# Kernel optimization log

Measured on AMD Instinct MI355X. Metric: run time of the kernel, lower is better.

The kernel has to match this reference:

```python
import jax, jax.numpy as jnp
import numpy as np


def _block(x, a, b):
    # [..., W, H, D] -> [..., W//a, H//b, a, b, D]
    w, h, d = x.shape[-3:]
    x = jnp.reshape(x, x.shape[:-3] + (w // a, a, h // b, b, d))
    return jnp.moveaxis(x, -4, -3)


def _combine(x, bs):
    # [..., W, H, D] -> [..., W//bs, H//bs, bs*bs*D]
    x = _block(x, bs, bs)
    return jnp.reshape(x, x.shape[:-3] + (-1,))


def _normalize(x):
    x = x - jnp.mean(x, axis=-1, keepdims=True)
    return x / (jnp.linalg.norm(x, axis=-1, keepdims=True) + 1e-05)


def setup_inputs() -> dict:
    key = jax.random.key(0)
    k1, k2 = jax.random.split(key)
    x = jax.random.normal(k1, (8, 128, 128, 64), dtype=jnp.float32)
    y = jax.random.normal(k2, (8, 128, 128, 64), dtype=jnp.float32)
    return {"x": x, "y": y, "blocksize": 4}


def reference(x, y, blocksize):
    shape = x.shape
    xc = _normalize(_combine(x, blocksize))  # [B, W/bs, H/bs, F]
    yc = _normalize(_combine(y, blocksize))
    yf = jnp.reshape(yc, (-1, yc.shape[-1]))  # [M, F] codebook
    # single similarity matrix, reused for min-loss and argmax (original
    # computed jnp.inner twice -- same math)
    sim = jnp.einsum('...f,mf->...m', xc, yf)  # [B, W/bs, H/bs, M]
    cosloss = jnp.mean(jnp.min(1.0 - sim, axis=-1))
    idx = jnp.argmax(sim, axis=-1)
    # one-hot matmul against yf == top-1 gather (argmax picks first max, as
    # does the original I = (argmax - arange == 0) construction)
    new_x = jnp.take(yf, idx, axis=0)  # [B, W/bs, H/bs, F]
    new_x = jnp.reshape(new_x, new_x.shape[:-1] + (blocksize, blocksize, -1))
    new_x = jnp.swapaxes(new_x, -4, -3)
    new_x = jnp.reshape(new_x, shape)
    return cosloss, new_x
```

## Files before the change

kernel.cpp:

```cpp
#include <hip/hip_runtime.h>
#include <math.h>


#define NROWS 8192
#define KY 1024
#define NCH 32
#define EPS 3e-4f
#define FEPS 8e-4f

typedef _Float16 v8h __attribute__((ext_vector_type(8)));
typedef float f32x4 __attribute__((ext_vector_type(4)));

__device__ __forceinline__ void gload16(const _Float16* g, _Float16* l) {
    __builtin_amdgcn_global_load_lds(
        (const __attribute__((address_space(1))) void*)g,
        (__attribute__((address_space(3))) void*)l, 16, 0, 0);
}

__device__ __forceinline__ unsigned umax(unsigned a, unsigned b) { return a > b ? a : b; }
__device__ __forceinline__ unsigned umin(unsigned a, unsigned b) { return a < b ? a : b; }

__device__ __forceinline__ unsigned packKey(float v, int col) {
    unsigned b = __float_as_uint(v);
    b ^= (unsigned)((int)b >> 31) | 0x80000000u;
    return (b & 0xFFFFE000u) | (unsigned)(8191 - col);
}

__device__ __forceinline__ float unpackApprox(unsigned k) {
    unsigned kb = k & 0xFFFFE000u;
    unsigned b = (kb & 0x80000000u) ? (kb ^ 0x80000000u) : ~kb;
    return __uint_as_float(b);
}

#define KMERGE(a1, a2, a3, b1, b2, b3) do {                                 \
    unsigned _n1 = umax(a1, b1);                                            \
    unsigned _n2 = umax(umin(a1, b1), umax(a2, b2));                        \
    unsigned _n3 = umax(umax(a3, b3), umax(umin(a1, b2), umin(a2, b1)));    \
    a1 = _n1; a2 = _n2; a3 = _n3;                                           \
} while (0)

__global__ __launch_bounds__(256) void normSplitKernel(
    const float* __restrict__ x, const float* __restrict__ y,
    _Float16* __restrict__ Xh, _Float16* __restrict__ Xl,
    _Float16* __restrict__ Yh, _Float16* __restrict__ Yl,
    int* __restrict__ flagCnt) {
    if (blockIdx.x == 0 && threadIdx.x == 0) *flagCnt = 0;
    int gr = blockIdx.x * 4 + (threadIdx.x >> 6);
    int ln = threadIdx.x & 63;
    bool isX = gr < NROWS;
    int row = isX ? gr : gr - NROWS;
    const float* src = isX ? x : y;
    _Float16* dh = isX ? Xh : Yh;
    _Float16* dl = isX ? Xl : Yl;
    int b = row >> 10, wq = (row >> 5) & 31, hq = row & 31;
    int a = ln >> 4, c = (ln >> 2) & 3, d0 = (ln & 3) << 4;
    const float* p = &src[(((size_t)(b * 128) + wq * 4 + a) * 128 + hq * 4 + c) * 64 + d0];
    float vv[16];
    *(float4*)(vv + 0)  = *(const float4*)(p + 0);
    *(float4*)(vv + 4)  = *(const float4*)(p + 4);
    *(float4*)(vv + 8)  = *(const float4*)(p + 8);
    *(float4*)(vv + 12) = *(const float4*)(p + 12);
    double s = 0.0;
    #pragma unroll
    for (int q = 0; q < 16; q++) s += (double)vv[q];
    #pragma unroll
    for (int m = 1; m < 64; m <<= 1) s += __shfl_xor(s, m, 64);
    double mean = s * (1.0 / 1024.0);
    double ss = 0.0;
    #pragma unroll
    for (int q = 0; q < 16; q++) {
        double d = (double)vv[q] - mean;
        ss += d * d;
    }
    #pragma unroll
    for (int m = 1; m < 64; m <<= 1) ss += __shfl_xor(ss, m, 64);
    double scale = 1.0 / (sqrt(ss) + 1e-5);
    _Float16 hi[16], lo[16];
    #pragma unroll
    for (int q = 0; q < 16; q++) {
        float f = (float)(((double)vv[q] - mean) * scale);
        _Float16 h = (_Float16)f;
        hi[q] = h;
        lo[q] = (_Float16)(f - (float)h);
    }
    size_t f0 = (size_t)row * KY + (ln << 4);
    *(v8h*)&dh[f0]     = *(v8h*)(hi);
    *(v8h*)&dh[f0 + 8] = *(v8h*)(hi + 8);
    *(v8h*)&dl[f0]     = *(v8h*)(lo);
    *(v8h*)&dl[f0 + 8] = *(v8h*)(lo + 8);
}

__global__ __launch_bounds__(512, 2) void simKernel(
    const _Float16* __restrict__ Xh, const _Float16* __restrict__ Yh,
    float* __restrict__ pV1, unsigned* __restrict__ pK1,
    unsigned* __restrict__ pK2, unsigned* __restrict__ pK3) {
    __shared__ __align__(16) _Float16 As[2][256 * 32];
    __shared__ __align__(16) _Float16 Bs[2][256 * 32];
    __shared__ unsigned sK[2][4][128][3];
    __shared__ float sE[2][4][128];
    const int t = threadIdx.x;
    const int l = t & 63, w = t >> 6;
    const int wr = w >> 2, wc = w & 3;
    const int quad = l >> 4, lm = l & 15;
    const int flat = blockIdx.x;
    const int bx = flat >> 5, by = flat & 31;
    const int r0 = bx * 256, c0 = by * 256;

    f32x4 acc[8][4];
    #pragma unroll
    for (int i = 0; i < 8; i++)
        #pragma unroll
        for (int j = 0; j < 4; j++) acc[i][j] = (f32x4){0.f, 0.f, 0.f, 0.f};

    const int cq = l >> 2;
    const int sA = (((l & 3) ^ (cq & 3)) << 3);
    const _Float16* gA = Xh + (size_t)(r0 + w * 16 + cq) * KY + sA;
    const _Float16* gB = Yh + (size_t)(c0 + w * 16 + cq) * KY + sA;
    const int ldsBase = w * 512;

#define STAGE(bb, kt) do {                                             \
    const int _ko = (kt) * 32;                                         \
    gload16(gA + _ko,                     &As[bb][ldsBase]);           \
    gload16(gA + _ko + (size_t)128 * KY,  &As[bb][ldsBase + 4096]);    \
    gload16(gB + _ko,                     &Bs[bb][ldsBase]);           \
    gload16(gB + _ko + (size_t)128 * KY,  &Bs[bb][ldsBase + 4096]);    \
} while (0)

    const int swz = (quad ^ (lm & 3)) << 3;
    const int offA0 = (wr * 128 + lm) * 32 + swz;
    const int offB0 = (wc * 64 + lm) * 32 + swz;

    STAGE(0, 0);
    STAGE(1, 1);
    asm volatile("s_waitcnt vmcnt(4)" ::: "memory");
    __builtin_amdgcn_s_barrier();

    #pragma unroll 2
    for (int kt = 0; kt < 32; kt++) {
        const int cur = kt & 1;
        v8h af[8], bf[4];
        #pragma unroll
        for (int i = 0; i < 8; i++) af[i] = *(const v8h*)&As[cur][offA0 + i * 512];
        #pragma unroll
        for (int j = 0; j < 4; j++) bf[j] = *(const v8h*)&Bs[cur][offB0 + j * 512];
        asm volatile("s_waitcnt lgkmcnt(0)" ::: "memory");
        __builtin_amdgcn_sched_barrier(0);
        __builtin_amdgcn_s_barrier();
        STAGE(cur, (kt + 2) & 31);
        __builtin_amdgcn_s_setprio(1);
        #pragma unroll
        for (int j = 0; j < 4; j++)
            #pragma unroll
            for (int i = 0; i < 8; i++)
                acc[i][j] = __builtin_amdgcn_mfma_f32_16x16x32_f16(af[i], bf[j], acc[i][j], 0, 0, 0);
        __builtin_amdgcn_s_setprio(0);
        asm volatile("s_waitcnt vmcnt(4)" ::: "memory");
        __builtin_amdgcn_s_barrier();
    }
    asm volatile("s_waitcnt vmcnt(0)" ::: "memory");
#undef STAGE

    const int cbase = c0 + wc * 64 + lm;
    #pragma unroll
    for (int i = 0; i < 8; i++) {
        #pragma unroll
        for (int r = 0; r < 4; r++) {
            float v0 = acc[i][0][r], v1 = acc[i][1][r];
            float v2 = acc[i][2][r], v3 = acc[i][3][r];
            unsigned k0 = packKey(v0, cbase);
            unsigned k1 = packKey(v1, cbase + 16);
            unsigned k2 = packKey(v2, cbase + 32);
            unsigned k3 = packKey(v3, cbase + 48);
            unsigned h1 = umax(k0, k1), l1 = umin(k0, k1);
            unsigned h2 = umax(k2, k3), l2 = umin(k2, k3);
            unsigned a1 = umax(h1, h2);
            unsigned a2 = umax(umin(h1, h2), umax(l1, l2));
            unsigned a3 = umax(umin(h1, l2), umin(l1, h2));
            float ev = fmaxf(fmaxf(v0, v1), fmaxf(v2, v3));
            #pragma unroll
            for (int m = 1; m < 16; m <<= 1) {
                unsigned b1 = (unsigned)__shfl_xor((int)a1, m, 64);
                unsigned b2 = (unsigned)__shfl_xor((int)a2, m, 64);
                unsigned b3 = (unsigned)__shfl_xor((int)a3, m, 64);
                float be = __shfl_xor(ev, m, 64);
                KMERGE(a1, a2, a3, b1, b2, b3);
                ev = fmaxf(ev, be);
            }
            if (lm == 0) {
                int rr = i * 16 + quad * 4 + r;
                sK[wr][wc][rr][0] = a1; sK[wr][wc][rr][1] = a2; sK[wr][wc][rr][2] = a3;
                sE[wr][wc][rr] = ev;
            }
        }
    }
    __syncthreads();
    if (t < 256) {
        const int mwr = t >> 7, ri = t & 127;
        unsigned a1 = sK[mwr][0][ri][0], a2 = sK[mwr][0][ri][1], a3 = sK[mwr][0][ri][2];
        float ev = sE[mwr][0][ri];
        #pragma unroll
        for (int q = 1; q < 4; q++) {
            unsigned b1 = sK[mwr][q][ri][0], b2 = sK[mwr][q][ri][1], b3 = sK[mwr][q][ri][2];
            KMERGE(a1, a2, a3, b1, b2, b3);
            ev = fmaxf(ev, sE[mwr][q][ri]);
        }
        size_t o = (size_t)by * NROWS + (r0 + t);
        pV1[o] = ev;
        pK1[o] = a1; pK2[o] = a2; pK3[o] = a3;
    }
}

__global__ __launch_bounds__(256) void reduceKernel(
    const float* __restrict__ pV1, const unsigned* __restrict__ pK1,
    const unsigned* __restrict__ pK2, const unsigned* __restrict__ pK3,
    int* __restrict__ bestIdx, int* __restrict__ flagRows,
    int* __restrict__ flagC2, int* __restrict__ flagC3,
    int* __restrict__ flagCnt, float* __restrict__ blkSum) {
    int t = threadIdx.x;
    int g = blockIdx.x * 256 + t;
    int row = g >> 2, sub = g & 3;
    unsigned a1 = 0, a2 = 0, a3 = 0;
    float ev = -1e30f;
    #pragma unroll
    for (int k = 0; k < 8; k++) {
        size_t o = (size_t)(sub + (k << 2)) * NROWS + row;
        unsigned b1 = pK1[o], b2 = pK2[o], b3 = pK3[o];
        float e = pV1[o];
        KMERGE(a1, a2, a3, b1, b2, b3);
        ev = fmaxf(ev, e);
    }
    #pragma unroll
    for (int m = 1; m < 4; m <<= 1) {
        unsigned b1 = (unsigned)__shfl_xor((int)a1, m, 64);
        unsigned b2 = (unsigned)__shfl_xor((int)a2, m, 64);
        unsigned b3 = (unsigned)__shfl_xor((int)a3, m, 64);
        float be = __shfl_xor(ev, m, 64);
        KMERGE(a1, a2, a3, b1, b2, b3);
        ev = fmaxf(ev, be);
    }
    bool lead = (t & 3) == 0;
    if (lead) {
        bestIdx[row] = 8191 - (int)(a1 & 8191u);
        if (ev - unpackApprox(a2) < FEPS) {
            int s = atomicAdd(flagCnt, 1);
            flagRows[s] = row;
            flagC2[s] = 8191 - (int)(a2 & 8191u);
            flagC3[s] = 8191 - (int)(a3 & 8191u);
        }
    }
    double sum = lead ? 1.0 - (double)ev : 0.0;
    __shared__ double sh[4];
    #pragma unroll
    for (int off = 32; off; off >>= 1) sum += __shfl_down(sum, off, 64);
    if ((t & 63) == 0) sh[t >> 6] = sum;
    __syncthreads();
    if (t == 0) blkSum[blockIdx.x] = (float)(sh[0] + sh[1] + sh[2] + sh[3]);
}

__global__ __launch_bounds__(256) void refineKernel(
    const _Float16* __restrict__ Xh, const _Float16* __restrict__ Xl,
    const _Float16* __restrict__ Yh, const _Float16* __restrict__ Yl,
    int* __restrict__ bestIdx, const int* __restrict__ flagRows,
    const int* __restrict__ flagC2, const int* __restrict__ flagC3,
    const int* __restrict__ flagCnt) {
    int n = *flagCnt;
    int wave = (blockIdx.x << 2) + (threadIdx.x >> 6);
    int ln = threadIdx.x & 63;
    for (int fi = wave; fi < n; fi += gridDim.x * 4) {
        int row = flagRows[fi];
        int cand[3];
        cand[0] = bestIdx[row]; cand[1] = flagC2[fi]; cand[2] = flagC3[fi];
        double d[3];
        #pragma unroll
        for (int c = 0; c < 3; c++) {
            double p = 0.0;
            int yr = cand[c];
            #pragma unroll
            for (int q = 0; q < 16; q++) {
                int k = (ln << 4) + q;
                float xv = (float)Xh[(size_t)row * KY + k] + (float)Xl[(size_t)row * KY + k];
                float yv = (float)Yh[(size_t)yr * KY + k] + (float)Yl[(size_t)yr * KY + k];
                p += (double)xv * yv;
            }
            #pragma unroll
            for (int m = 1; m < 64; m <<= 1) p += __shfl_xor(p, m, 64);
            d[c] = p;
        }
        if (ln == 0) {
            int bi = cand[0]; double bv = d[0];
            #pragma unroll
            for (int c = 1; c < 3; c++) {
                if (d[c] > bv || (d[c] == bv && cand[c] < bi)) { bv = d[c]; bi = cand[c]; }
            }
            bestIdx[row] = bi;
        }
    }
}

__global__ __launch_bounds__(256) void gatherKernel(
    const _Float16* __restrict__ Yh, const _Float16* __restrict__ Yl,
    const int* __restrict__ bestIdx, const float* __restrict__ blkSum,
    float* __restrict__ out) {
    int t = threadIdx.x;
    if (blockIdx.x == 0 && t == 0) {
        double s = 0.0;
        for (int i = 0; i < 128; i++) s += (double)blkSum[i];
        out[0] = (float)(s / 8192.0);
    }
    int g = (blockIdx.x * 256 + t) << 2;
    int b = g >> 20, wq = (g >> 13) & 127, hq = (g >> 6) & 127, d = g & 63;
    int row = (b << 10) + ((wq >> 2) << 5) + (hq >> 2);
    int f = ((wq & 3) << 8) + ((hq & 3) << 6) + d;
    size_t base = (size_t)bestIdx[row] * KY + f;
    const _Float16* ph = &Yh[base];
    const _Float16* pl = &Yl[base];
    out[1 + g + 0] = (float)ph[0] + (float)pl[0];
    out[1 + g + 1] = (float)ph[1] + (float)pl[1];
    out[1 + g + 2] = (float)ph[2] + (float)pl[2];
    out[1 + g + 3] = (float)ph[3] + (float)pl[3];
}

extern "C" void kernel_launch(void* const* d_in, const int* in_sizes, int n_in,
                              void* d_out, int out_size, void* d_ws, size_t ws_size,
                              hipStream_t stream) {
    const float* x = (const float*)d_in[0];
    const float* y = (const float*)d_in[1];
    float* out = (float*)d_out;
    char* ws = (char*)d_ws;
    _Float16* Xh  = (_Float16*)(ws);
    _Float16* Xl  = (_Float16*)(ws + 16777216u);
    _Float16* Yh  = (_Float16*)(ws + 33554432u);
    _Float16* Yl  = (_Float16*)(ws + 50331648u);
    float* pV1    = (float*)(ws + 67108864u);
    unsigned* pK1 = (unsigned*)(ws + 69206016u);
    unsigned* pK2 = (unsigned*)(ws + 71303168u);
    unsigned* pK3 = (unsigned*)(ws + 73400320u);
    int* bestIdx  = (int*)  (ws + 79691776u);
    int* flagRows = (int*)  (ws + 79724544u);
    int* flagC2   = (int*)  (ws + 79757312u);
    int* flagC3   = (int*)  (ws + 79790080u);
    int* flagCnt  = (int*)  (ws + 79822848u);
    float* blkSum = (float*)(ws + 79822976u);

    normSplitKernel<<<4096, 256, 0, stream>>>(x, y, Xh, Xl, Yh, Yl, flagCnt);
    simKernel<<<1024, 512, 0, stream>>>(Xh, Yh, pV1, pK1, pK2, pK3);
    reduceKernel<<<128, 256, 0, stream>>>(pV1, pK1, pK2, pK3,
                                          bestIdx, flagRows, flagC2, flagC3, flagCnt, blkSum);
    refineKernel<<<64, 256, 0, stream>>>(Xh, Xl, Yh, Yl, bestIdx,
                                         flagRows, flagC2, flagC3, flagCnt);
    gatherKernel<<<8192, 256, 0, stream>>>(Yh, Yl, bestIdx, blkSum, out);
}
```

Baseline: 328.8 us.

## Double K-tile depth to 64 and restructure LDS prefetch pipeline

The similarity GEMM now stages 64-wide K slices, up from 32, into double-buffered LDS with a new 8-way XOR swizzle. The loop shrinks from 32 to 16 iterations. Each iteration issues the next tile's global-to-LDS loads first, runs two MFMA sub-steps, then waits and barriers once. This halves the number of barriers and waitcnt stalls per K, but doubles LDS use to about 156KB per block. It also replaces the two-tile-ahead prefetch with one tile ahead, which may expose more memory latency.

```diff
diff --git a/kernel.cpp b/kernel.cpp
--- a/kernel.cpp
+++ b/kernel.cpp
@@ -94,8 +94,8 @@
     const _Float16* __restrict__ Xh, const _Float16* __restrict__ Yh,
     float* __restrict__ pV1, unsigned* __restrict__ pK1,
     unsigned* __restrict__ pK2, unsigned* __restrict__ pK3) {
-    __shared__ __align__(16) _Float16 As[2][256 * 32];
-    __shared__ __align__(16) _Float16 Bs[2][256 * 32];
+    __shared__ __align__(16) _Float16 As[2][256 * 64];
+    __shared__ __align__(16) _Float16 Bs[2][256 * 64];
     __shared__ unsigned sK[2][4][128][3];
     __shared__ float sE[2][4][128];
     const int t = threadIdx.x;
@@ -112,52 +112,60 @@
         #pragma unroll
         for (int j = 0; j < 4; j++) acc[i][j] = (f32x4){0.f, 0.f, 0.f, 0.f};
 
-    const int cq = l >> 2;
-    const int sA = (((l & 3) ^ (cq & 3)) << 3);
-    const _Float16* gA = Xh + (size_t)(r0 + w * 16 + cq) * KY + sA;
-    const _Float16* gB = Yh + (size_t)(c0 + w * 16 + cq) * KY + sA;
-    const int ldsBase = w * 512;
-
-#define STAGE(bb, kt) do {                                             \
-    const int _ko = (kt) * 32;                                         \
-    gload16(gA + _ko,                     &As[bb][ldsBase]);           \
-    gload16(gA + _ko + (size_t)128 * KY,  &As[bb][ldsBase + 4096]);    \
-    gload16(gB + _ko,                     &Bs[bb][ldsBase]);           \
-    gload16(gB + _ko + (size_t)128 * KY,  &Bs[bb][ldsBase + 4096]);    \
+    const int lh = l >> 3, ll = l & 7;
+    const int srow = w * 8 + lh;
+    const int scol = (ll ^ lh) << 3;
+    const _Float16* gA0 = Xh + (size_t)(r0 + srow) * KY + scol;
+    const _Float16* gB0 = Yh + (size_t)(c0 + srow) * KY + scol;
+    const int ldsS = w * 512;
+
+#define STAGE(bb, kt) do {                                                   \
+    const size_t _ko = (size_t)(kt) * 64;                                    \
+    gload16(gA0 + _ko,                       &As[bb][ldsS]);                 \
+    gload16(gB0 + _ko,                       &Bs[bb][ldsS]);                 \
+    gload16(gA0 + (size_t)64  * KY + _ko,    &As[bb][4096 + ldsS]);          \
+    gload16(gB0 + (size_t)64  * KY + _ko,    &Bs[bb][4096 + ldsS]);          \
+    gload16(gA0 + (size_t)128 * KY + _ko,    &As[bb][8192 + ldsS]);          \
+    gload16(gB0 + (size_t)128 * KY + _ko,    &Bs[bb][8192 + ldsS]);          \
+    gload16(gA0 + (size_t)192 * KY + _ko,    &As[bb][12288 + ldsS]);         \
+    gload16(gB0 + (size_t)192 * KY + _ko,    &Bs[bb][12288 + ldsS]);         \
 } while (0)
 
-    const int swz = (quad ^ (lm & 3)) << 3;
-    const int offA0 = (wr * 128 + lm) * 32 + swz;
-    const int offB0 = (wc * 64 + lm) * 32 + swz;
+    const int arow = (wr * 128 + lm) * 64;
+    const int brow = (wc * 64 + lm) * 64;
+    const int sw7 = lm & 7;
 
     STAGE(0, 0);
-    STAGE(1, 1);
-    asm volatile("s_waitcnt vmcnt(4)" ::: "memory");
+    asm volatile("s_waitcnt vmcnt(0)" ::: "memory");
     __builtin_amdgcn_s_barrier();
-
-    #pragma unroll 2
-    for (int kt = 0; kt < 32; kt++) {
+    __builtin_amdgcn_sched_barrier(0);
+
+    #pragma unroll 1
+    for (int kt = 0; kt < 16; kt++) {
         const int cur = kt & 1;
-        v8h af[8], bf[4];
-        #pragma unroll
-        for (int i = 0; i < 8; i++) af[i] = *(const v8h*)&As[cur][offA0 + i * 512];
-        #pragma unroll
-        for (int j = 0; j < 4; j++) bf[j] = *(const v8h*)&Bs[cur][offB0 + j * 512];
-        asm volatile("s_waitcnt lgkmcnt(0)" ::: "memory");
+        STAGE(cur ^ 1, (kt + 1) & 15);
+        #pragma unroll
+        for (int ks = 0; ks < 2; ks++) {
+            const int cA = ((ks * 4 + quad) ^ sw7) << 3;
+            v8h af[8], bf[4];
+            #pragma unroll
+            for (int i = 0; i < 8; i++)
+                af[i] = *(const v8h*)&As[cur][arow + i * 1024 + cA];
+            #pragma unroll
+            for (int j = 0; j < 4; j++)
+                bf[j] = *(const v8h*)&Bs[cur][brow + j * 1024 + cA];
+            __builtin_amdgcn_s_setprio(1);
+            #pragma unroll
+            for (int j = 0; j < 4; j++)
+                #pragma unroll
+                for (int i = 0; i < 8; i++)
+                    acc[i][j] = __builtin_amdgcn_mfma_f32_16x16x32_f16(af[i], bf[j], acc[i][j], 0, 0, 0);
+            __builtin_amdgcn_s_setprio(0);
+        }
+        asm volatile("s_waitcnt vmcnt(0)" ::: "memory");
+        __builtin_amdgcn_s_barrier();
         __builtin_amdgcn_sched_barrier(0);
-        __builtin_amdgcn_s_barrier();
-        STAGE(cur, (kt + 2) & 31);
-        __builtin_amdgcn_s_setprio(1);
-        #pragma unroll
-        for (int j = 0; j < 4; j++)
-            #pragma unroll
-            for (int i = 0; i < 8; i++)
-                acc[i][j] = __builtin_amdgcn_mfma_f32_16x16x32_f16(af[i], bf[j], acc[i][j], 0, 0, 0);
-        __builtin_amdgcn_s_setprio(0);
-        asm volatile("s_waitcnt vmcnt(4)" ::: "memory");
-        __builtin_amdgcn_s_barrier();
-    }
-    asm volatile("s_waitcnt vmcnt(0)" ::: "memory");
+    }
 #undef STAGE
 
     const int cbase = c0 + wc * 64 + lm;
```

After: 320.7 us. -2.5%, faster.
